# Kernel optimization log

Hardware: AMD Instinct MI355X
Metric: run time of the kernel (lower is better)

The kernel has to match this reference:

```python
import jax, jax.numpy as jnp
import numpy as np

N_NODES = 50000
N_EDGES = 800000
IN_DIM = 256
HEADS = 4
HEAD_DIM = 64  # out_dim // heads
NEG_SLOPE = 0.2  # PyG GATConv default


def setup_inputs() -> dict:
    key = jax.random.key(0)
    k1, k2, k3, k4, k5 = jax.random.split(key, 5)
    x = jax.random.normal(k1, (N_NODES, IN_DIM), dtype=jnp.float32)
    edge_index = jax.random.randint(k2, (2, N_EDGES), 0, N_NODES, dtype=jnp.int64)
    # Glorot-ish scaling
    W = jax.random.normal(k3, (IN_DIM, HEADS * HEAD_DIM), dtype=jnp.float32) * (1.0 / np.sqrt(IN_DIM))
    att_src = jax.random.normal(k4, (HEADS, HEAD_DIM), dtype=jnp.float32) * (1.0 / np.sqrt(HEAD_DIM))
    att_dst = jax.random.normal(k5, (HEADS, HEAD_DIM), dtype=jnp.float32) * (1.0 / np.sqrt(HEAD_DIM))
    bias = jnp.zeros((HEADS * HEAD_DIM,), dtype=jnp.float32)
    return {"x": x, "edge_index": edge_index, "W": W, "att_src": att_src,
            "att_dst": att_dst, "bias": bias}


def reference(x, edge_index, W, att_src, att_dst, bias):
    N = x.shape[0]
    # add self-loops (PyG GATConv default)
    loops = jnp.arange(N, dtype=edge_index.dtype)
    src = jnp.concatenate([edge_index[0], loops])
    dst = jnp.concatenate([edge_index[1], loops])

    h = (x @ W).reshape(N, HEADS, HEAD_DIM)          # [N,H,D]
    a_src = jnp.einsum('nhd,hd->nh', h, att_src)     # [N,H]
    a_dst = jnp.einsum('nhd,hd->nh', h, att_dst)     # [N,H]

    e = a_src[src] + a_dst[dst]                      # [E,H]
    e = jax.nn.leaky_relu(e, NEG_SLOPE)

    # segment softmax over edges sharing a destination node
    m = jax.ops.segment_max(e, dst, num_segments=N)  # [N,H]
    e = jnp.exp(e - m[dst])
    denom = jax.ops.segment_sum(e, dst, num_segments=N)  # [N,H]
    alpha = e / denom[dst]                           # [E,H]

    msg = alpha[:, :, None] * h[src]                 # [E,H,D]
    out = jax.ops.segment_sum(msg, dst, num_segments=N)  # [N,H,D]
    return out.reshape(N, HEADS * HEAD_DIM) + bias
```

## Files before the change

### kernel.cpp

```cpp
#include <hip/hip_runtime.h>
#include <hip/hip_bf16.h>

#define N_NODES 50000
#define N_EDGES 800000
#define IN_DIM 256
#define HEADS 4
#define HEAD_DIM 64
#define OUT_DIM 256
#define NEG_SLOPE 0.2f
#define TOTAL_E (N_EDGES + N_NODES)
#define M_PAD 50048
#define SEG_CAP 64

#define GEMM_BLOCKS 782
#define SCAT_BLOCKS 3321
#define MEGA_BLOCKS (GEMM_BLOCKS + SCAT_BLOCKS)

typedef float floatx4 __attribute__((ext_vector_type(4)));
typedef short shortx8 __attribute__((ext_vector_type(8)));

__global__ __launch_bounds__(256) void prep(const float* __restrict__ W,
                                            ushort* __restrict__ Wt,
                                            int* __restrict__ cnt) {
    int b = blockIdx.x;
    if (b < 64) {
        int t = b * 256 + threadIdx.x;
        int n = t >> 6;
        int k = (t & 63) << 2;
        ushort4 o;
        o.x = __bfloat16_as_ushort(__float2bfloat16(W[(size_t)(k + 0) * OUT_DIM + n]));
        o.y = __bfloat16_as_ushort(__float2bfloat16(W[(size_t)(k + 1) * OUT_DIM + n]));
        o.z = __bfloat16_as_ushort(__float2bfloat16(W[(size_t)(k + 2) * OUT_DIM + n]));
        o.w = __bfloat16_as_ushort(__float2bfloat16(W[(size_t)(k + 3) * OUT_DIM + n]));
        *(ushort4*)&Wt[(size_t)n * IN_DIM + k] = o;
    } else {
        int t = (b - 64) * 256 + threadIdx.x;
        if (t < 12500) ((int4*)cnt)[t] = make_int4(0, 0, 0, 0);
    }
}
#define PREP_BLOCKS 113

__global__ __launch_bounds__(256) void mega_kernel(const float* __restrict__ x,
                                                   const ushort* __restrict__ Wt,
                                                   const float* __restrict__ att_src,
                                                   const float* __restrict__ att_dst,
                                                   const int* __restrict__ e_src,
                                                   const int* __restrict__ e_dst,
                                                   int* __restrict__ cnt,
                                                   int* __restrict__ csr,
                                                   ushort* __restrict__ h2,
                                                   float* __restrict__ asrc,
                                                   float* __restrict__ adst) {
    __shared__ float A_lds[2][64 * 32];

    if (blockIdx.x >= GEMM_BLOCKS) {
        int id = (blockIdx.x - GEMM_BLOCKS) * 256 + threadIdx.x;
        if (id < N_EDGES) {
            int s = e_src[id];
            int dn = e_dst[id];
            int pos = atomicAdd(&cnt[dn], 1);
            if (pos < SEG_CAP) csr[(dn << 6) + pos] = s;
        } else if (id < TOTAL_E) {
            int nn = id - N_EDGES;
            int pos = atomicAdd(&cnt[nn], 1);
            if (pos < SEG_CAP) csr[(nn << 6) + pos] = nn;
        }
        return;
    }

    const int tid = threadIdx.x;
    const int w = tid >> 6;
    const int lane = tid & 63;
    const int quad = lane >> 4;
    const int l16 = lane & 15;
    const int row0 = blockIdx.x * 64;

    auto stage = [&](int buf, int k0) {
#pragma unroll
        for (int i = 0; i < 2; ++i) {
            int s = i * 256 + tid;
            int row = s >> 3;
            int cg = (s & 7) ^ (row & 7);
            int gr = row0 + row;
            if (gr > N_NODES - 1) gr = N_NODES - 1;
            const float* src = &x[(size_t)gr * IN_DIM + k0 + cg * 4];
            __builtin_amdgcn_global_load_lds(
                (const __attribute__((address_space(1))) unsigned int*)src,
                (__attribute__((address_space(3))) unsigned int*)&A_lds[buf][s * 4],
                16, 0, 0);
        }
    };

    floatx4 acc[4][4] = {};
    const ushort* wtb = Wt + (size_t)(w * 64 + l16) * IN_DIM + quad * 8;

    stage(0, 0);
    __syncthreads();
#pragma unroll 2
    for (int t = 0; t < 8; ++t) {
        int cur = t & 1;
        if (t < 7) stage(cur ^ 1, (t + 1) * 32);
        int k0 = t * 32;
        shortx8 bfr[4], af[4];
#pragma unroll
        for (int c = 0; c < 4; ++c)
            bfr[c] = *(const shortx8*)(wtb + (size_t)c * 16 * IN_DIM + k0);
#pragma unroll
        for (int r = 0; r < 4; ++r) {
            int row = r * 16 + l16;
            const float* Ab = &A_lds[cur][row * 32];
            int sw = row & 7;
            float4 f0 = *(const float4*)&Ab[((2 * quad) ^ sw) * 4];
            float4 f1 = *(const float4*)&Ab[((2 * quad + 1) ^ sw) * 4];
            float f[8] = {f0.x, f0.y, f0.z, f0.w, f1.x, f1.y, f1.z, f1.w};
            alignas(16) ushort a8[8];
#pragma unroll
            for (int u = 0; u < 8; ++u)
                a8[u] = __bfloat16_as_ushort(__float2bfloat16(f[u]));
            af[r] = *(const shortx8*)a8;
        }
#pragma unroll
        for (int r = 0; r < 4; ++r)
#pragma unroll
            for (int c = 0; c < 4; ++c)
                acc[r][c] = __builtin_amdgcn_mfma_f32_16x16x32_bf16(bfr[c], af[r],
                                                                    acc[r][c], 0, 0, 0);
        __syncthreads();
    }

    float as_cj[16], ad_cj[16];
#pragma unroll
    for (int c = 0; c < 4; ++c)
#pragma unroll
        for (int j = 0; j < 4; ++j) {
            int col = w * 64 + c * 16 + quad * 4 + j;
            as_cj[c * 4 + j] = att_src[col];
            ad_cj[c * 4 + j] = att_dst[col];
        }
#pragma unroll
    for (int r = 0; r < 4; ++r) {
        float s = 0.f, d = 0.f;
        alignas(16) ushort o16[16];
#pragma unroll
        for (int c = 0; c < 4; ++c)
#pragma unroll
            for (int j = 0; j < 4; ++j) {
                float v = acc[r][c][j];
                s = fmaf(v, as_cj[c * 4 + j], s);
                d = fmaf(v, ad_cj[c * 4 + j], d);
                o16[c * 4 + j] = __bfloat16_as_ushort(__float2bfloat16(v));
            }
        s += __shfl_xor(s, 16);
        s += __shfl_xor(s, 32);
        d += __shfl_xor(d, 16);
        d += __shfl_xor(d, 32);
        int gr = row0 + r * 16 + l16;
        if (quad == 0 && gr < N_NODES) {
            asrc[gr * HEADS + w] = s;
            adst[gr * HEADS + w] = d;
        }
        ushort* hp = h2 + (size_t)gr * OUT_DIM + w * 64 + quad * 16;
        *(uint4*)hp = *(const uint4*)&o16[0];
        *(uint4*)(hp + 8) = *(const uint4*)&o16[8];
    }
}

__global__ __launch_bounds__(256) void aggregate_v8(const uint2* __restrict__ h2,
                                                    const float* __restrict__ a_src,
                                                    const float* __restrict__ a_dst,
                                                    const int* __restrict__ cnt,
                                                    const int* __restrict__ csr,
                                                    const float* __restrict__ bias,
                                                    float* __restrict__ out) {
    int n = blockIdx.x * 4 + (threadIdx.x >> 6);
    if (n >= N_NODES) return;
    int lane = threadIdx.x & 63;
    int h = lane >> 4;
    int col0 = ((lane >> 4) << 6) + ((lane & 3) << 4) + (((lane >> 2) & 3) << 2);
    int beg = n << 6;
    int cn = min(cnt[n], SEG_CAP);
    int nfull = cn >> 3, rem = cn & 7;
    float adv = a_dst[n * HEADS + h];

    float den = 0.f;
    float acc0 = 0.f, acc1 = 0.f, acc2 = 0.f, acc3 = 0.f;
    for (int b = 0; b < nfull; ++b) {
        int i = beg + b * 8;
        int4 sa = *(const int4*)&csr[i];
        int4 sb = *(const int4*)&csr[i + 4];
        int ss[8] = {sa.x, sa.y, sa.z, sa.w, sb.x, sb.y, sb.z, sb.w};
        float asv[8];
        uint2 hv[8];
#pragma unroll
        for (int u = 0; u < 8; ++u) {
            asv[u] = a_src[ss[u] * HEADS + h];
            hv[u] = h2[(size_t)ss[u] * 64 + lane];
        }
#pragma unroll
        for (int u = 0; u < 8; ++u) {
            float e = asv[u] + adv;
            e = fmaxf(e, NEG_SLOPE * e);
            float p = __expf(e);
            den += p;
            acc0 = fmaf(p, __uint_as_float(hv[u].x << 16), acc0);
            acc1 = fmaf(p, __uint_as_float(hv[u].x & 0xffff0000u), acc1);
            acc2 = fmaf(p, __uint_as_float(hv[u].y << 16), acc2);
            acc3 = fmaf(p, __uint_as_float(hv[u].y & 0xffff0000u), acc3);
        }
    }
    if (rem) {
        int i = beg + nfull * 8;
        int4 sa = *(const int4*)&csr[i];
        int4 sb = *(const int4*)&csr[i + 4];
        int ss[8] = {sa.x, sa.y, sa.z, sa.w, sb.x, sb.y, sb.z, sb.w};
        float asv[8];
        uint2 hv[8];
#pragma unroll
        for (int u = 0; u < 8; ++u) {
            int s = (u < rem) ? ss[u] : 0;
            asv[u] = a_src[s * HEADS + h];
            hv[u] = h2[(size_t)s * 64 + lane];
        }
#pragma unroll
        for (int u = 0; u < 8; ++u) {
            float e = asv[u] + adv;
            e = fmaxf(e, NEG_SLOPE * e);
            float p = (u < rem) ? __expf(e) : 0.f;
            den += p;
            acc0 = fmaf(p, __uint_as_float(hv[u].x << 16), acc0);
            acc1 = fmaf(p, __uint_as_float(hv[u].x & 0xffff0000u), acc1);
            acc2 = fmaf(p, __uint_as_float(hv[u].y << 16), acc2);
            acc3 = fmaf(p, __uint_as_float(hv[u].y & 0xffff0000u), acc3);
        }
    }
    float idv = 1.0f / den;
    float4 b = *(const float4*)&bias[col0];
    float4 o = make_float4(acc0 * idv + b.x, acc1 * idv + b.y,
                           acc2 * idv + b.z, acc3 * idv + b.w);
    *(float4*)&out[(size_t)n * OUT_DIM + col0] = o;
}

extern "C" void kernel_launch(void* const* d_in, const int* in_sizes, int n_in,
                              void* d_out, int out_size, void* d_ws, size_t ws_size,
                              hipStream_t stream) {
    const float* x = (const float*)d_in[0];
    const int* ei = (const int*)d_in[1];
    const float* W = (const float*)d_in[2];
    const float* att_src = (const float*)d_in[3];
    const float* att_dst = (const float*)d_in[4];
    const float* bias = (const float*)d_in[5];
    float* out = (float*)d_out;

    const int* e_src = ei;
    const int* e_dst = ei + N_EDGES;

    char* p = (char*)d_ws;
    auto alloc = [&](size_t bytes) {
        void* r = (void*)p;
        p += (bytes + 255) & ~(size_t)255;
        return r;
    };
    ushort* h2   = (ushort*)alloc((size_t)M_PAD * OUT_DIM * 2);
    float* asrc  = (float*)alloc((size_t)N_NODES * HEADS * 4);
    float* adst  = (float*)alloc((size_t)N_NODES * HEADS * 4);
    int* cnt     = (int*)alloc((size_t)N_NODES * 4);
    int* csr     = (int*)alloc((size_t)N_NODES * SEG_CAP * 4);
    ushort* Wt   = (ushort*)alloc((size_t)IN_DIM * OUT_DIM * 2);

    prep<<<PREP_BLOCKS, 256, 0, stream>>>(W, Wt, cnt);
    mega_kernel<<<MEGA_BLOCKS, 256, 0, stream>>>(x, Wt, att_src, att_dst, e_src, e_dst,
                                                 cnt, csr, h2, asrc, adst);
    aggregate_v8<<<(N_NODES + 3) / 4, 256, 0, stream>>>((const uint2*)h2, asrc, adst,
                                                        cnt, csr, bias, out);
}
```

Measured before the change: 226.4 us.

## Vectorize edge scatter, drop LDS swizzle, and deepen GEMM prefetch pipeline

The scatter blocks now handle four edges per thread with int4 loads, which cuts the scatter block count by four. The GEMM staging drops the XOR swizzle on the A tile in LDS. The k-loop is rewritten to keep two stages in flight, using explicit vmcnt waits and raw s_barrier instead of __syncthreads, and is fully unrolled. The goal is more overlap between global loads and MFMA work and fewer scatter threads. Removing the swizzle risks LDS bank conflicts on the float4 reads, and the hand-placed waitcnts are easy to get wrong.

```diff
diff --git a/kernel.cpp b/kernel.cpp
--- a/kernel.cpp
+++ b/kernel.cpp
@@ -13,7 +13,9 @@
 #define SEG_CAP 64
 
 #define GEMM_BLOCKS 782
-#define SCAT_BLOCKS 3321
+#define EDGE_VT 200000
+#define SCAT_VT 212500
+#define SCAT_BLOCKS 831
 #define MEGA_BLOCKS (GEMM_BLOCKS + SCAT_BLOCKS)
 
 typedef float floatx4 __attribute__((ext_vector_type(4)));
@@ -54,16 +56,26 @@
     __shared__ float A_lds[2][64 * 32];
 
     if (blockIdx.x >= GEMM_BLOCKS) {
-        int id = (blockIdx.x - GEMM_BLOCKS) * 256 + threadIdx.x;
-        if (id < N_EDGES) {
-            int s = e_src[id];
-            int dn = e_dst[id];
-            int pos = atomicAdd(&cnt[dn], 1);
-            if (pos < SEG_CAP) csr[(dn << 6) + pos] = s;
-        } else if (id < TOTAL_E) {
-            int nn = id - N_EDGES;
-            int pos = atomicAdd(&cnt[nn], 1);
-            if (pos < SEG_CAP) csr[(nn << 6) + pos] = nn;
+        int t = (blockIdx.x - GEMM_BLOCKS) * 256 + threadIdx.x;
+        if (t < EDGE_VT) {
+            int4 s4 = ((const int4*)e_src)[t];
+            int4 d4 = ((const int4*)e_dst)[t];
+            int ss[4] = {s4.x, s4.y, s4.z, s4.w};
+            int dd[4] = {d4.x, d4.y, d4.z, d4.w};
+            int pos[4];
+#pragma unroll
+            for (int u = 0; u < 4; ++u) pos[u] = atomicAdd(&cnt[dd[u]], 1);
+#pragma unroll
+            for (int u = 0; u < 4; ++u)
+                if (pos[u] < SEG_CAP) csr[(dd[u] << 6) + pos[u]] = ss[u];
+        } else if (t < SCAT_VT) {
+            int n0 = (t - EDGE_VT) * 4;
+            int pos[4];
+#pragma unroll
+            for (int u = 0; u < 4; ++u) pos[u] = atomicAdd(&cnt[n0 + u], 1);
+#pragma unroll
+            for (int u = 0; u < 4; ++u)
+                if (pos[u] < SEG_CAP) csr[((n0 + u) << 6) + pos[u]] = n0 + u;
         }
         return;
     }
@@ -80,10 +92,9 @@
         for (int i = 0; i < 2; ++i) {
             int s = i * 256 + tid;
             int row = s >> 3;
-            int cg = (s & 7) ^ (row & 7);
             int gr = row0 + row;
             if (gr > N_NODES - 1) gr = N_NODES - 1;
-            const float* src = &x[(size_t)gr * IN_DIM + k0 + cg * 4];
+            const float* src = &x[(size_t)gr * IN_DIM + k0 + (s & 7) * 4];
             __builtin_amdgcn_global_load_lds(
                 (const __attribute__((address_space(1))) unsigned int*)src,
                 (__attribute__((address_space(3))) unsigned int*)&A_lds[buf][s * 4],
@@ -95,23 +106,23 @@
     const ushort* wtb = Wt + (size_t)(w * 64 + l16) * IN_DIM + quad * 8;
 
     stage(0, 0);
-    __syncthreads();
-#pragma unroll 2
+    stage(1, 32);
+    asm volatile("s_waitcnt vmcnt(2)" ::: "memory");
+    __builtin_amdgcn_s_barrier();
+
+#pragma unroll
     for (int t = 0; t < 8; ++t) {
-        int cur = t & 1;
-        if (t < 7) stage(cur ^ 1, (t + 1) * 32);
-        int k0 = t * 32;
+        const int cur = t & 1;
+        const int k0 = t * 32;
         shortx8 bfr[4], af[4];
 #pragma unroll
         for (int c = 0; c < 4; ++c)
             bfr[c] = *(const shortx8*)(wtb + (size_t)c * 16 * IN_DIM + k0);
 #pragma unroll
         for (int r = 0; r < 4; ++r) {
-            int row = r * 16 + l16;
-            const float* Ab = &A_lds[cur][row * 32];
-            int sw = row & 7;
-            float4 f0 = *(const float4*)&Ab[((2 * quad) ^ sw) * 4];
-            float4 f1 = *(const float4*)&Ab[((2 * quad + 1) ^ sw) * 4];
+            const float* Ab = &A_lds[cur][(r * 16 + l16) * 32 + quad * 8];
+            float4 f0 = *(const float4*)Ab;
+            float4 f1 = *(const float4*)(Ab + 4);
             float f[8] = {f0.x, f0.y, f0.z, f0.w, f1.x, f1.y, f1.z, f1.w};
             alignas(16) ushort a8[8];
 #pragma unroll
@@ -125,7 +136,16 @@
             for (int c = 0; c < 4; ++c)
                 acc[r][c] = __builtin_amdgcn_mfma_f32_16x16x32_bf16(bfr[c], af[r],
                                                                     acc[r][c], 0, 0, 0);
-        __syncthreads();
+        if (t == 7) break;
+        asm volatile("s_waitcnt lgkmcnt(0)" ::: "memory");
+        __builtin_amdgcn_s_barrier();
+        if (t < 6) {
+            stage(cur, (t + 2) * 32);
+            asm volatile("s_waitcnt vmcnt(2)" ::: "memory");
+        } else {
+            asm volatile("s_waitcnt vmcnt(0)" ::: "memory");
+        }
+        __builtin_amdgcn_s_barrier();
     }
 
     float as_cj[16], ad_cj[16];
```

Result: slower. 237.5 us (+4.9%).

## Split mega kernel into separate scatter and GEMM launches, prefill self-loops in prep

Applied to the files above, without the earlier changes.

The fused kernel that ran GEMM blocks and edge-scatter blocks side by side is split into a scatter kernel and a GEMM kernel launched one after the other. Self-loop entries are now written in prep, which initializes the counts to 1 and stores each node's own index in slot 0, so the scatter no longer does atomics for self-loops. This trades the concurrency of the fused launch for simpler, more homogeneous kernels and one extra launch. Self-loops now always occupy slot 0 of each segment instead of a racy position.

```diff
diff --git a/kernel.cpp b/kernel.cpp
--- a/kernel.cpp
+++ b/kernel.cpp
@@ -8,20 +8,20 @@
 #define HEAD_DIM 64
 #define OUT_DIM 256
 #define NEG_SLOPE 0.2f
-#define TOTAL_E (N_EDGES + N_NODES)
 #define M_PAD 50048
 #define SEG_CAP 64
 
 #define GEMM_BLOCKS 782
-#define SCAT_BLOCKS 3321
-#define MEGA_BLOCKS (GEMM_BLOCKS + SCAT_BLOCKS)
+#define SCAT_BLOCKS 3125
+#define PREP_BLOCKS 260
 
 typedef float floatx4 __attribute__((ext_vector_type(4)));
 typedef short shortx8 __attribute__((ext_vector_type(8)));
 
 __global__ __launch_bounds__(256) void prep(const float* __restrict__ W,
                                             ushort* __restrict__ Wt,
-                                            int* __restrict__ cnt) {
+                                            int* __restrict__ cnt,
+                                            int* __restrict__ csr) {
     int b = blockIdx.x;
     if (b < 64) {
         int t = b * 256 + threadIdx.x;
@@ -35,38 +35,32 @@
         *(ushort4*)&Wt[(size_t)n * IN_DIM + k] = o;
     } else {
         int t = (b - 64) * 256 + threadIdx.x;
-        if (t < 12500) ((int4*)cnt)[t] = make_int4(0, 0, 0, 0);
-    }
-}
-#define PREP_BLOCKS 113
-
-__global__ __launch_bounds__(256) void mega_kernel(const float* __restrict__ x,
+        if (t < N_NODES) csr[t << 6] = t;
+        if (t < 12500) ((int4*)cnt)[t] = make_int4(1, 1, 1, 1);
+    }
+}
+
+__global__ __launch_bounds__(256) void scatter_kernel(const int* __restrict__ e_src,
+                                                      const int* __restrict__ e_dst,
+                                                      int* __restrict__ cnt,
+                                                      int* __restrict__ csr) {
+    int id = blockIdx.x * 256 + threadIdx.x;
+    if (id < N_EDGES) {
+        int s = e_src[id];
+        int d = e_dst[id];
+        int pos = atomicAdd(&cnt[d], 1);
+        if (pos < SEG_CAP) csr[(d << 6) + pos] = s;
+    }
+}
+
+__global__ __launch_bounds__(256) void gemm_kernel(const float* __restrict__ x,
                                                    const ushort* __restrict__ Wt,
                                                    const float* __restrict__ att_src,
                                                    const float* __restrict__ att_dst,
-                                                   const int* __restrict__ e_src,
-                                                   const int* __restrict__ e_dst,
-                                                   int* __restrict__ cnt,
-                                                   int* __restrict__ csr,
                                                    ushort* __restrict__ h2,
                                                    float* __restrict__ asrc,
                                                    float* __restrict__ adst) {
     __shared__ float A_lds[2][64 * 32];
-
-    if (blockIdx.x >= GEMM_BLOCKS) {
-        int id = (blockIdx.x - GEMM_BLOCKS) * 256 + threadIdx.x;
-        if (id < N_EDGES) {
-            int s = e_src[id];
-            int dn = e_dst[id];
-            int pos = atomicAdd(&cnt[dn], 1);
-            if (pos < SEG_CAP) csr[(dn << 6) + pos] = s;
-        } else if (id < TOTAL_E) {
-            int nn = id - N_EDGES;
-            int pos = atomicAdd(&cnt[nn], 1);
-            if (pos < SEG_CAP) csr[(nn << 6) + pos] = nn;
-        }
-        return;
-    }
 
     const int tid = threadIdx.x;
     const int w = tid >> 6;
@@ -107,9 +101,9 @@
             bfr[c] = *(const shortx8*)(wtb + (size_t)c * 16 * IN_DIM + k0);
 #pragma unroll
         for (int r = 0; r < 4; ++r) {
-            int row = r * 16 + l16;
+            const int row = r * 16 + l16;
+            const int sw = row & 7;
             const float* Ab = &A_lds[cur][row * 32];
-            int sw = row & 7;
             float4 f0 = *(const float4*)&Ab[((2 * quad) ^ sw) * 4];
             float4 f1 = *(const float4*)&Ab[((2 * quad + 1) ^ sw) * 4];
             float f[8] = {f0.x, f0.y, f0.z, f0.w, f1.x, f1.y, f1.z, f1.w};
@@ -267,9 +261,9 @@
     int* csr     = (int*)alloc((size_t)N_NODES * SEG_CAP * 4);
     ushort* Wt   = (ushort*)alloc((size_t)IN_DIM * OUT_DIM * 2);
 
-    prep<<<PREP_BLOCKS, 256, 0, stream>>>(W, Wt, cnt);
-    mega_kernel<<<MEGA_BLOCKS, 256, 0, stream>>>(x, Wt, att_src, att_dst, e_src, e_dst,
-                                                 cnt, csr, h2, asrc, adst);
+    prep<<<PREP_BLOCKS, 256, 0, stream>>>(W, Wt, cnt, csr);
+    scatter_kernel<<<SCAT_BLOCKS, 256, 0, stream>>>(e_src, e_dst, cnt, csr);
+    gemm_kernel<<<GEMM_BLOCKS, 256, 0, stream>>>(x, Wt, att_src, att_dst, h2, asrc, adst);
     aggregate_v8<<<(N_NODES + 3) / 4, 256, 0, stream>>>((const uint2*)h2, asrc, adst,
                                                         cnt, csr, bias, out);
 }
```

Measured after the change: 246.8 us. 1.09x slower.
